# Optimization experiments

Measured on AMD Instinct MI355X. Metric: run time of the kernel, lower is better.

Reference implementation:

```python
import jax, jax.numpy as jnp
import numpy as np

N_NODES = 10000
N_EDGES = 4096
IN_F = 300
OUT_F = 150


def setup_inputs() -> dict:
    key = jax.random.key(0)
    ks = jax.random.split(key, 7)
    features = jax.random.normal(ks[0], (N_NODES, IN_F), dtype=jnp.float32)
    efeat = jax.random.normal(ks[1], (N_EDGES, 1), dtype=jnp.float32)
    # edge_func: Linear(1, IN_F*OUT_F) producing per-edge weight matrices
    W_edge = jax.random.normal(ks[2], (1, IN_F * OUT_F), dtype=jnp.float32) * (1.0)
    b_edge = jax.random.normal(ks[3], (IN_F * OUT_F,), dtype=jnp.float32) * 0.02
    bias = jax.random.normal(ks[4], (OUT_F,), dtype=jnp.float32) * 0.02
    src = jax.random.randint(ks[5], (N_EDGES,), 0, N_NODES, dtype=jnp.int32)
    dst = jax.random.randint(ks[6], (N_EDGES,), 0, N_NODES, dtype=jnp.int32)
    return {"features": features, "efeat": efeat, "W_edge": W_edge,
            "b_edge": b_edge, "bias": bias, "src": src, "dst": dst}


def reference(features, efeat, W_edge, b_edge, bias, src, dst):
    # edge_func: Linear on edge features -> per-edge weight matrix [E, IN_F, OUT_F]
    We = (efeat @ W_edge + b_edge).reshape(-1, IN_F, OUT_F)
    # gather source node features and apply per-edge matmul: m_e = h_src[e] @ W_e
    h_src = features[src]                       # [E, IN_F]
    msgs = jnp.einsum('ei,eio->eo', h_src, We)  # [E, OUT_F]
    # scatter-mean to destination nodes
    sums = jax.ops.segment_sum(msgs, dst, num_segments=N_NODES)          # [N, OUT_F]
    cnts = jax.ops.segment_sum(jnp.ones((msgs.shape[0],), msgs.dtype), dst,
                               num_segments=N_NODES)                     # [N]
    mean = sums / jnp.maximum(cnts, 1.0)[:, None]  # nodes w/o in-edges -> 0
    return jax.nn.relu(mean + bias)
```

## Files before the change

kernel.cpp:

```cpp
#include <hip/hip_runtime.h>

#define NNODES 10000
#define NEDGES 4096
#define INF 300
#define OUTF 150
#define EPB 16
#define NGROUPS (NEDGES / EPB)
#define SPLITK 6
#define KCHUNK (INF / SPLITK)
#define EDGE_THREADS 192

__global__ __launch_bounds__(EDGE_THREADS) void edge_msg_kernel(
    const float* __restrict__ feat, const float* __restrict__ efeat,
    const float* __restrict__ W, const float* __restrict__ B,
    const int* __restrict__ src, const int* __restrict__ dst,
    float* __restrict__ sums, float* __restrict__ cnts)
{
    __shared__ float hA[EPB][KCHUNK];
    __shared__ float s_ef[EPB];
    __shared__ int   s_dst[EPB];
    __shared__ int   s_src[EPB];

    const int tid = threadIdx.x;
    const int kc  = blockIdx.x / NGROUPS;
    const int grp = blockIdx.x - kc * NGROUPS;
    const int e0  = grp * EPB;
    const int k0  = kc * KCHUNK;

    if (tid < EPB) {
        const int e = e0 + tid;
        s_src[tid] = src[e];
        s_dst[tid] = dst[e];
        s_ef[tid]  = efeat[e];
    }
    __syncthreads();

    for (int idx = tid; idx < EPB * KCHUNK; idx += EDGE_THREADS) {
        const int el = idx / KCHUNK;
        const int i  = idx - el * KCHUNK;
        hA[el][i] = feat[(long)s_src[el] * INF + k0 + i];
    }
    __syncthreads();

    if (tid < OUTF) {
        float accW[EPB], accB[EPB];
        #pragma unroll
        for (int e = 0; e < EPB; ++e) { accW[e] = 0.f; accB[e] = 0.f; }

        const float* Wc = W + (long)k0 * OUTF + tid;
        const float* Bc = B + (long)k0 * OUTF + tid;
        #pragma unroll 2
        for (int i = 0; i < KCHUNK; ++i) {
            const float w  = Wc[(long)i * OUTF];
            const float bv = Bc[(long)i * OUTF];
            #pragma unroll
            for (int e = 0; e < EPB; ++e) {
                const float h = hA[e][i];
                accW[e] = fmaf(h, w,  accW[e]);
                accB[e] = fmaf(h, bv, accB[e]);
            }
        }
        #pragma unroll
        for (int e = 0; e < EPB; ++e) {
            const float msg = fmaf(s_ef[e], accW[e], accB[e]);
            atomicAdd(&sums[(long)s_dst[e] * OUTF + tid], msg);
        }
    } else if (kc == 0 && tid < OUTF + EPB) {
        atomicAdd(&cnts[s_dst[tid - OUTF]], 1.0f);
    }
}

__global__ __launch_bounds__(256) void finalize_kernel(
    const float* __restrict__ sums, const float* __restrict__ cnts,
    const float* __restrict__ bias, float* __restrict__ out)
{
    const int idx = blockIdx.x * blockDim.x + threadIdx.x;
    const int total = NNODES * OUTF;
    if (idx < total) {
        const int n = idx / OUTF;
        const int o = idx - n * OUTF;
        const float c = cnts[n];
        const float m = sums[idx] / fmaxf(c, 1.0f);
        const float v = m + bias[o];
        out[idx] = v > 0.f ? v : 0.f;
    }
}

extern "C" void kernel_launch(void* const* d_in, const int* in_sizes, int n_in,
                              void* d_out, int out_size, void* d_ws, size_t ws_size,
                              hipStream_t stream) {
    const float* feat  = (const float*)d_in[0];
    const float* efeat = (const float*)d_in[1];
    const float* W     = (const float*)d_in[2];
    const float* B     = (const float*)d_in[3];
    const float* bias  = (const float*)d_in[4];
    const int*   src   = (const int*)d_in[5];
    const int*   dst   = (const int*)d_in[6];
    float* out  = (float*)d_out;

    float* sums = (float*)d_ws;
    float* cnts = sums + (size_t)NNODES * OUTF;

    hipMemsetAsync(d_ws, 0, ((size_t)NNODES * OUTF + NNODES) * sizeof(float), stream);

    edge_msg_kernel<<<NGROUPS * SPLITK, EDGE_THREADS, 0, stream>>>(
        feat, efeat, W, B, src, dst, sums, cnts);

    const int total = NNODES * OUTF;
    finalize_kernel<<<(total + 255) / 256, 256, 0, stream>>>(sums, cnts, bias, out);
}
```

Measured before the change: 111.8 us.

## Fold edge scalar into features and concatenate W and B into one K=600 GEMM

The two per-edge accumulators (W and B paths) are merged into a single contraction. The efeat scale is folded into a doubled feature row, and W and B are concatenated into one 600x150 matrix built by a new prep kernel. That same prep kernel also replaces the memset by zeroing the workspace. Edges per block grow to 32 and split-K to 15, feature loads use float4, and the inner loop is unrolled by 4 over k. This halves the register accumulators and reuses each weight load across more edges, at the cost of an extra kernel that copies W and B every call and more atomics from the higher split-K.

```diff
diff --git a/kernel.cpp b/kernel.cpp
--- a/kernel.cpp
+++ b/kernel.cpp
@@ -4,15 +4,33 @@
 #define NEDGES 4096
 #define INF 300
 #define OUTF 150
-#define EPB 16
+#define KCAT (2 * INF)
+#define EPB 32
 #define NGROUPS (NEDGES / EPB)
-#define SPLITK 6
-#define KCHUNK (INF / SPLITK)
-#define EDGE_THREADS 192
+#define SPLITK 15
+#define KCHUNK (KCAT / SPLITK)
+#define ETHREADS 192
 
-__global__ __launch_bounds__(EDGE_THREADS) void edge_msg_kernel(
+#define SUMS_N   (NNODES * OUTF)
+#define ZERO_N   (SUMS_N + NNODES)
+#define WCAT_N   (KCAT * OUTF)
+
+__global__ __launch_bounds__(256) void prep_kernel(
+    const float* __restrict__ W, const float* __restrict__ B,
+    float* __restrict__ zero_region, float* __restrict__ wcat)
+{
+    const int idx = blockIdx.x * blockDim.x + threadIdx.x;
+    if (idx < ZERO_N) {
+        zero_region[idx] = 0.f;
+    } else if (idx < ZERO_N + WCAT_N) {
+        const int j = idx - ZERO_N;
+        wcat[j] = (j < INF * OUTF) ? W[j] : B[j - INF * OUTF];
+    }
+}
+
+__global__ __launch_bounds__(ETHREADS) void edge_msg_kernel(
     const float* __restrict__ feat, const float* __restrict__ efeat,
-    const float* __restrict__ W, const float* __restrict__ B,
+    const float* __restrict__ wcat,
     const int* __restrict__ src, const int* __restrict__ dst,
     float* __restrict__ sums, float* __restrict__ cnts)
 {
@@ -35,36 +53,43 @@
     }
     __syncthreads();
 
-    for (int idx = tid; idx < EPB * KCHUNK; idx += EDGE_THREADS) {
-        const int el = idx / KCHUNK;
-        const int i  = idx - el * KCHUNK;
-        hA[el][i] = feat[(long)s_src[el] * INF + k0 + i];
+    for (int q = tid; q < EPB * (KCHUNK / 4); q += ETHREADS) {
+        const int el = q / (KCHUNK / 4);
+        const int j4 = q - el * (KCHUNK / 4);
+        const int gi = k0 + 4 * j4;
+        const float* rp = feat + (size_t)s_src[el] * INF;
+        float4 v;
+        if (gi < INF) {
+            v = *(const float4*)(rp + gi);
+            const float ef = s_ef[el];
+            v.x *= ef; v.y *= ef; v.z *= ef; v.w *= ef;
+        } else {
+            v = *(const float4*)(rp + gi - INF);
+        }
+        *(float4*)&hA[el][4 * j4] = v;
     }
     __syncthreads();
 
     if (tid < OUTF) {
-        float accW[EPB], accB[EPB];
+        float acc[EPB];
         #pragma unroll
-        for (int e = 0; e < EPB; ++e) { accW[e] = 0.f; accB[e] = 0.f; }
+        for (int e = 0; e < EPB; ++e) acc[e] = 0.f;
 
-        const float* Wc = W + (long)k0 * OUTF + tid;
-        const float* Bc = B + (long)k0 * OUTF + tid;
-        #pragma unroll 2
-        for (int i = 0; i < KCHUNK; ++i) {
-            const float w  = Wc[(long)i * OUTF];
-            const float bv = Bc[(long)i * OUTF];
+        const float* Wc = wcat + (size_t)k0 * OUTF + tid;
+        for (int i4 = 0; i4 < KCHUNK; i4 += 4) {
+            const float w0 = Wc[(size_t)(i4 + 0) * OUTF];
+            const float w1 = Wc[(size_t)(i4 + 1) * OUTF];
+            const float w2 = Wc[(size_t)(i4 + 2) * OUTF];
+            const float w3 = Wc[(size_t)(i4 + 3) * OUTF];
             #pragma unroll
             for (int e = 0; e < EPB; ++e) {
-                const float h = hA[e][i];
-                accW[e] = fmaf(h, w,  accW[e]);
-                accB[e] = fmaf(h, bv, accB[e]);
+                const float4 h = *(const float4*)&hA[e][i4];
+                acc[e] = fmaf(h.w, w3, fmaf(h.z, w2, fmaf(h.y, w1, fmaf(h.x, w0, acc[e]))));
             }
         }
         #pragma unroll
-        for (int e = 0; e < EPB; ++e) {
-            const float msg = fmaf(s_ef[e], accW[e], accB[e]);
-            atomicAdd(&sums[(long)s_dst[e] * OUTF + tid], msg);
-        }
+        for (int e = 0; e < EPB; ++e)
+            atomicAdd(&sums[(size_t)s_dst[e] * OUTF + tid], acc[e]);
     } else if (kc == 0 && tid < OUTF + EPB) {
         atomicAdd(&cnts[s_dst[tid - OUTF]], 1.0f);
     }
@@ -75,8 +100,7 @@
     const float* __restrict__ bias, float* __restrict__ out)
 {
     const int idx = blockIdx.x * blockDim.x + threadIdx.x;
-    const int total = NNODES * OUTF;
-    if (idx < total) {
+    if (idx < SUMS_N) {
         const int n = idx / OUTF;
         const int o = idx - n * OUTF;
         const float c = cnts[n];
@@ -99,13 +123,14 @@
     float* out  = (float*)d_out;
 
     float* sums = (float*)d_ws;
-    float* cnts = sums + (size_t)NNODES * OUTF;
+    float* cnts = sums + SUMS_N;
+    float* wcat = sums + ZERO_N;
 
-    hipMemsetAsync(d_ws, 0, ((size_t)NNODES * OUTF + NNODES) * sizeof(float), stream);
+    const int prep_total = ZERO_N + WCAT_N;
+    prep_kernel<<<(prep_total + 255) / 256, 256, 0, stream>>>(W, B, sums, wcat);
 
-    edge_msg_kernel<<<NGROUPS * SPLITK, EDGE_THREADS, 0, stream>>>(
-        feat, efeat, W, B, src, dst, sums, cnts);
+    edge_msg_kernel<<<NGROUPS * SPLITK, ETHREADS, 0, stream>>>(
+        feat, efeat, wcat, src, dst, sums, cnts);
 
-    const int total = NNODES * OUTF;
-    finalize_kernel<<<(total + 255) / 256, 256, 0, stream>>>(sums, cnts, bias, out);
+    finalize_kernel<<<(SUMS_N + 255) / 256, 256, 0, stream>>>(sums, cnts, bias, out);
 }
```

New measurement: 138.6 us. 24.0% more time.
